# Performance work log

Hardware: AMD Instinct MI355X
Metric: run time of the kernel (lower is better)

The kernel has to match this reference:

```python
import jax, jax.numpy as jnp
import numpy as np

B, S, H, I, C = 1024, 512, 128, 1, 10


def _uniform(key, shape, fan):
    stdv = 1.0 / np.sqrt(fan)
    return jax.random.uniform(key, shape, jnp.float32, -stdv, stdv)


def setup_inputs() -> dict:
    key = jax.random.key(0)
    ks = jax.random.split(key, 16)
    return {
        "x": jax.random.normal(ks[0], (B, S), jnp.float32),
        "W_gx": _uniform(ks[1], (I, H), H),
        "W_gh": _uniform(ks[2], (H, H), H),
        "W_ix": _uniform(ks[3], (I, H), H),
        "W_ih": _uniform(ks[4], (H, H), H),
        "W_fx": _uniform(ks[5], (I, H), H),
        "W_fh": _uniform(ks[6], (H, H), H),
        "W_ox": _uniform(ks[7], (I, H), H),
        "W_oh": _uniform(ks[8], (H, H), H),
        "W_ph": _uniform(ks[9], (H, C), C),
        "b_g": _uniform(ks[10], (H,), 1),
        "b_i": _uniform(ks[11], (H,), 1),
        "b_f": _uniform(ks[12], (H,), 1),
        "b_o": _uniform(ks[13], (H,), 1),
        "b_p": _uniform(ks[14], (C,), 1),
    }


def reference(x, W_gx, W_gh, W_ix, W_ih, W_fx, W_fh, W_ox, W_oh, W_ph,
              b_g, b_i, b_f, b_o, b_p):
    Hd = W_gh.shape[0]
    # Fuse the four per-gate GEMMs into one (same math, concatenated weights).
    Wx = jnp.concatenate([W_gx, W_ix, W_fx, W_ox], axis=1)   # [I, 4H]
    Wh = jnp.concatenate([W_gh, W_ih, W_fh, W_oh], axis=1)   # [H, 4H]
    b = jnp.concatenate([b_g, b_i, b_f, b_o])                # [4H]
    # input_dim == 1: timestep t input is x[:, t:t+1] -> xs: [S, B, 1]
    xs = jnp.swapaxes(x[:, :, None], 0, 1)
    # Precompute all input projections in one big GEMM: [S, B, 4H]
    xp = xs @ Wx + b

    def step(carry, xp_t):
        h, c = carry
        gates = xp_t + h @ Wh                    # [B, 4H]
        g = jnp.tanh(gates[:, :Hd])
        i = jax.nn.sigmoid(gates[:, Hd:2 * Hd])
        f = jax.nn.sigmoid(gates[:, 2 * Hd:3 * Hd])
        o = jax.nn.sigmoid(gates[:, 3 * Hd:])
        c_t = g * i + c * f
        h_t = jnp.tanh(c_t) * o
        return (h_t, c_t), None

    h0 = jnp.zeros((x.shape[0], Hd), x.dtype)
    (h_last, _), _ = jax.lax.scan(step, (h0, h0), xp)
    return h_last @ W_ph + b_p                   # logits at final timestep
```

## Files before the change

kernel.cpp:

```cpp
#include <hip/hip_runtime.h>

#define S_LEN 512
#define H_DIM 128
#define C_DIM 10

typedef __attribute__((ext_vector_type(8))) short short8;
typedef __attribute__((ext_vector_type(4))) float f32x4;

__device__ __forceinline__ unsigned short f2bf(float f) {
    union { float f; unsigned u; } v; v.f = f;
    return (unsigned short)((v.u + 0x7FFFu + ((v.u >> 16) & 1u)) >> 16);
}

__device__ __forceinline__ float fast_sigmoid(float x) {
    float e = __builtin_amdgcn_exp2f(-1.4426950408889634f * x);
    return __builtin_amdgcn_rcpf(1.0f + e);
}
__device__ __forceinline__ float fast_tanh(float x) {
    float e = __builtin_amdgcn_exp2f(2.8853900817779268f * x);
    return 1.0f - 2.0f * __builtin_amdgcn_rcpf(e + 1.0f);
}

__global__ __launch_bounds__(512, 1) void lstm_fused(
    const float* __restrict__ x,
    const float* __restrict__ Wgx, const float* __restrict__ Wgh,
    const float* __restrict__ Wix, const float* __restrict__ Wih,
    const float* __restrict__ Wfx, const float* __restrict__ Wfh,
    const float* __restrict__ Wox, const float* __restrict__ Woh,
    const float* __restrict__ Wph,
    const float* __restrict__ bg, const float* __restrict__ bi,
    const float* __restrict__ bff, const float* __restrict__ bo,
    const float* __restrict__ bp,
    float* __restrict__ out)
{
    __shared__ float xr[4][516];
    __shared__ __attribute__((aligned(16))) unsigned short hb[2][512];
    __shared__ float hfin[4][H_DIM];

    const int tid  = threadIdx.x;
    const int lane = tid & 63;
    const int w    = tid >> 6;
    const int b0   = blockIdx.x * 4;

    {
        const float* xp = x + b0 * S_LEN;
        #pragma unroll
        for (int r = 0; r < 4; ++r) xr[r][tid] = xp[r * S_LEN + tid];
    }
    ((unsigned short*)hb)[tid] = 0;

    const int jl = lane & 15;
    const int kg = lane >> 4;
    const int j  = w * 16 + jl;

    const float* WhA[4] = { Wgh, Wih, Wfh, Woh };
    short8 bfrag[4][4];
    #pragma unroll
    for (int g = 0; g < 4; ++g) {
        #pragma unroll
        for (int kk = 0; kk < 4; ++kk) {
            const float* src = WhA[g] + (kk * 32 + kg * 8) * H_DIM + j;
            short8 v;
            #pragma unroll
            for (int e = 0; e < 8; ++e) v[e] = (short)f2bf(src[e * H_DIM]);
            bfrag[g][kk] = v;
        }
    }
    const float wxv[4] = { Wgx[j], Wix[j], Wfx[j], Wox[j] };
    const float bv[4]  = { bg[j],  bi[j],  bff[j], bo[j]  };

    const int abase = ((lane & 15) >> 2) * 16 + (lane >> 4) * 64;
    const int widx  = kg * 8 + ((j >> 3) & 3) * 32 + (j >> 5) * 128 + (j & 7);

    float cst  = 0.f;
    float hcur = 0.f;
    const f32x4 zf = { 0.f, 0.f, 0.f, 0.f };

    __syncthreads();

    unsigned short* const h0 = &hb[0][0];
    unsigned short* const h1 = &hb[1][0];

    auto step = [&](const unsigned short* src, unsigned short* dst, float xv) {
        float seed[4];
        #pragma unroll
        for (int g = 0; g < 4; ++g) seed[g] = __builtin_fmaf(xv, wxv[g], bv[g]);

        const char* base = (const char*)src + abase;
        short8 afr[4];
        #pragma unroll
        for (int kk = 0; kk < 4; ++kk)
            afr[kk] = *(const short8*)(base + kk * 256);

        f32x4 r[4][4];
        #pragma unroll
        for (int kk = 0; kk < 4; ++kk)
            #pragma unroll
            for (int g = 0; g < 4; ++g)
                r[g][kk] = __builtin_amdgcn_mfma_f32_16x16x32_bf16(
                               afr[kk], bfrag[g][kk], zf, 0, 0, 0);

        float pre[4];
        #pragma unroll
        for (int g = 0; g < 4; ++g) {
            const float t01 = r[g][0][0] + r[g][1][0];
            const float t23 = r[g][2][0] + (r[g][3][0] + seed[g]);
            pre[g] = t01 + t23;
        }

        const float tg = fast_tanh(pre[0]);
        const float si = fast_sigmoid(pre[1]);
        const float sf = fast_sigmoid(pre[2]);
        const float so = fast_sigmoid(pre[3]);
        const float cn = __builtin_fmaf(cst, sf, tg * si);
        cst  = cn;
        const float hn = fast_tanh(cn) * so;
        hcur = hn;
        unsigned pk;
        asm("v_cvt_pk_bf16_f32 %0, %1, %2" : "=v"(pk) : "v"(hn), "v"(hn));
        dst[widx] = (unsigned short)pk;
        __syncthreads();
    };

    for (int t4 = 0; t4 < S_LEN; t4 += 4) {
        const f32x4 xq = *(const f32x4*)&xr[kg][t4];
        step(h0, h1, xq[0]);
        step(h1, h0, xq[1]);
        step(h0, h1, xq[2]);
        step(h1, h0, xq[3]);
    }

    hfin[kg][j] = hcur;
    __syncthreads();

    if (tid < 4 * C_DIM) {
        const int b = tid / C_DIM, cc = tid % C_DIM;
        float s = bp[cc];
        #pragma unroll 8
        for (int k = 0; k < H_DIM; ++k) s += hfin[b][k] * Wph[k * C_DIM + cc];
        out[(b0 + b) * C_DIM + cc] = s;
    }
}

extern "C" void kernel_launch(void* const* d_in, const int* in_sizes, int n_in,
                              void* d_out, int out_size, void* d_ws, size_t ws_size,
                              hipStream_t stream) {
    const float* x   = (const float*)d_in[0];
    const float* Wgx = (const float*)d_in[1];
    const float* Wgh = (const float*)d_in[2];
    const float* Wix = (const float*)d_in[3];
    const float* Wih = (const float*)d_in[4];
    const float* Wfx = (const float*)d_in[5];
    const float* Wfh = (const float*)d_in[6];
    const float* Wox = (const float*)d_in[7];
    const float* Woh = (const float*)d_in[8];
    const float* Wph = (const float*)d_in[9];
    const float* bg  = (const float*)d_in[10];
    const float* bi  = (const float*)d_in[11];
    const float* bf  = (const float*)d_in[12];
    const float* bo  = (const float*)d_in[13];
    const float* bp  = (const float*)d_in[14];
    float* out = (float*)d_out;

    lstm_fused<<<dim3(256), dim3(512), 0, stream>>>(
        x, Wgx, Wgh, Wix, Wih, Wfx, Wfh, Wox, Woh, Wph,
        bg, bi, bf, bo, bp, out);
}
```

Before: 252.8 us.

## Process two independent 4-row batch groups per block to interleave recurrences

Each block now handles 8 batch rows as two independent 4-row LSTM recurrences that share one barrier per timestep. Their MFMA chains and gate math are interleaved to hide latency, and the grid shrinks to 128 blocks. Only lanes with (lane&3)==0 load real A fragments and the rest keep zero fragments. This is meant to halve the number of barriers per batch row and raise instruction-level parallelism within a step. In exchange there is more register pressure and fewer blocks (128 on a 256-CU part), so some CUs sit idle.

After: 412.0 us. +63.0%, slower.

```diff
diff --git a/kernel.cpp b/kernel.cpp
--- a/kernel.cpp
+++ b/kernel.cpp
@@ -21,7 +21,7 @@
     return 1.0f - 2.0f * __builtin_amdgcn_rcpf(e + 1.0f);
 }
 
-__global__ __launch_bounds__(512, 1) void lstm_fused(
+__global__ __launch_bounds__(512, 2) void lstm_fused(
     const float* __restrict__ x,
     const float* __restrict__ Wgx, const float* __restrict__ Wgh,
     const float* __restrict__ Wix, const float* __restrict__ Wih,
@@ -33,21 +33,22 @@
     const float* __restrict__ bp,
     float* __restrict__ out)
 {
-    __shared__ float xr[4][516];
-    __shared__ __attribute__((aligned(16))) unsigned short hb[2][512];
-    __shared__ float hfin[4][H_DIM];
+    __shared__ float xr[8][516];
+    __shared__ __attribute__((aligned(16))) unsigned short hb[2][2][512];
+    __shared__ float hfin[8][H_DIM];
 
     const int tid  = threadIdx.x;
     const int lane = tid & 63;
     const int w    = tid >> 6;
-    const int b0   = blockIdx.x * 4;
+    const int b0   = blockIdx.x * 8;
 
     {
         const float* xp = x + b0 * S_LEN;
         #pragma unroll
-        for (int r = 0; r < 4; ++r) xr[r][tid] = xp[r * S_LEN + tid];
-    }
-    ((unsigned short*)hb)[tid] = 0;
+        for (int r = 0; r < 8; ++r) xr[r][tid] = xp[r * S_LEN + tid];
+    }
+    ((unsigned*)hb)[tid]       = 0;
+    ((unsigned*)hb)[tid + 512] = 0;
 
     const int jl = lane & 15;
     const int kg = lane >> 4;
@@ -69,71 +70,112 @@
     const float wxv[4] = { Wgx[j], Wix[j], Wfx[j], Wox[j] };
     const float bv[4]  = { bg[j],  bi[j],  bff[j], bo[j]  };
 
-    const int abase = ((lane & 15) >> 2) * 16 + (lane >> 4) * 64;
-    const int widx  = kg * 8 + ((j >> 3) & 3) * 32 + (j >> 5) * 128 + (j & 7);
-
-    float cst  = 0.f;
-    float hcur = 0.f;
-    const f32x4 zf = { 0.f, 0.f, 0.f, 0.f };
+    const bool aActive = (lane & 3) == 0;
+    const int  abase   = (lane >> 2) * 16;
+    const int  widx    = kg * 8 + ((j >> 3) & 3) * 32 + (j >> 5) * 128 + (j & 7);
+
+    float cst0 = 0.f, cst1 = 0.f;
+    float hcv0 = 0.f, hcv1 = 0.f;
+
+    short8 af0[4], af1[4];
+    #pragma unroll
+    for (int kk = 0; kk < 4; ++kk) {
+        af0[kk] = short8{0,0,0,0,0,0,0,0};
+        af1[kk] = short8{0,0,0,0,0,0,0,0};
+    }
 
     __syncthreads();
 
-    unsigned short* const h0 = &hb[0][0];
-    unsigned short* const h1 = &hb[1][0];
-
-    auto step = [&](const unsigned short* src, unsigned short* dst, float xv) {
-        float seed[4];
-        #pragma unroll
-        for (int g = 0; g < 4; ++g) seed[g] = __builtin_fmaf(xv, wxv[g], bv[g]);
-
-        const char* base = (const char*)src + abase;
-        short8 afr[4];
-        #pragma unroll
-        for (int kk = 0; kk < 4; ++kk)
-            afr[kk] = *(const short8*)(base + kk * 256);
-
-        f32x4 r[4][4];
-        #pragma unroll
-        for (int kk = 0; kk < 4; ++kk)
-            #pragma unroll
-            for (int g = 0; g < 4; ++g)
-                r[g][kk] = __builtin_amdgcn_mfma_f32_16x16x32_bf16(
-                               afr[kk], bfrag[g][kk], zf, 0, 0, 0);
-
-        float pre[4];
+    unsigned short* const g0a = &hb[0][0][0];
+    unsigned short* const g0b = &hb[0][1][0];
+    unsigned short* const g1a = &hb[1][0][0];
+    unsigned short* const g1b = &hb[1][1][0];
+
+    auto iter = [&](const unsigned short* s0, unsigned short* d0,
+                    const unsigned short* s1, unsigned short* d1,
+                    float xv0, float xv1) {
+        if (aActive) {
+            const char* base0 = (const char*)s0 + abase;
+            const char* base1 = (const char*)s1 + abase;
+            #pragma unroll
+            for (int kk = 0; kk < 4; ++kk) {
+                af0[kk] = *(const short8*)(base0 + kk * 256);
+                af1[kk] = *(const short8*)(base1 + kk * 256);
+            }
+        }
+        float seed0[4], seed1[4];
         #pragma unroll
         for (int g = 0; g < 4; ++g) {
-            const float t01 = r[g][0][0] + r[g][1][0];
-            const float t23 = r[g][2][0] + (r[g][3][0] + seed[g]);
-            pre[g] = t01 + t23;
-        }
-
-        const float tg = fast_tanh(pre[0]);
-        const float si = fast_sigmoid(pre[1]);
-        const float sf = fast_sigmoid(pre[2]);
-        const float so = fast_sigmoid(pre[3]);
-        const float cn = __builtin_fmaf(cst, sf, tg * si);
-        cst  = cn;
-        const float hn = fast_tanh(cn) * so;
-        hcur = hn;
-        unsigned pk;
-        asm("v_cvt_pk_bf16_f32 %0, %1, %2" : "=v"(pk) : "v"(hn), "v"(hn));
-        dst[widx] = (unsigned short)pk;
+            seed0[g] = __builtin_fmaf(xv0, wxv[g], bv[g]);
+            seed1[g] = __builtin_fmaf(xv1, wxv[g], bv[g]);
+        }
+
+        const f32x4 zf = { 0.f, 0.f, 0.f, 0.f };
+        f32x4 a00[4], a01[4], a10[4], a11[4];
+        #pragma unroll
+        for (int g = 0; g < 4; ++g) {
+            a00[g] = __builtin_amdgcn_mfma_f32_16x16x32_bf16(af0[0], bfrag[g][0], zf, 0, 0, 0);
+            a01[g] = __builtin_amdgcn_mfma_f32_16x16x32_bf16(af0[2], bfrag[g][2], zf, 0, 0, 0);
+            a10[g] = __builtin_amdgcn_mfma_f32_16x16x32_bf16(af1[0], bfrag[g][0], zf, 0, 0, 0);
+            a11[g] = __builtin_amdgcn_mfma_f32_16x16x32_bf16(af1[2], bfrag[g][2], zf, 0, 0, 0);
+        }
+        #pragma unroll
+        for (int g = 0; g < 4; ++g) {
+            a00[g] = __builtin_amdgcn_mfma_f32_16x16x32_bf16(af0[1], bfrag[g][1], a00[g], 0, 0, 0);
+            a01[g] = __builtin_amdgcn_mfma_f32_16x16x32_bf16(af0[3], bfrag[g][3], a01[g], 0, 0, 0);
+            a10[g] = __builtin_amdgcn_mfma_f32_16x16x32_bf16(af1[1], bfrag[g][1], a10[g], 0, 0, 0);
+            a11[g] = __builtin_amdgcn_mfma_f32_16x16x32_bf16(af1[3], bfrag[g][3], a11[g], 0, 0, 0);
+        }
+
+        {
+            float pre[4];
+            #pragma unroll
+            for (int g = 0; g < 4; ++g) pre[g] = a00[g][0] + (a01[g][0] + seed0[g]);
+            const float tg = fast_tanh(pre[0]);
+            const float si = fast_sigmoid(pre[1]);
+            const float sf = fast_sigmoid(pre[2]);
+            const float so = fast_sigmoid(pre[3]);
+            const float cn = __builtin_fmaf(cst0, sf, tg * si);
+            cst0 = cn;
+            const float hn = fast_tanh(cn) * so;
+            hcv0 = hn;
+            unsigned pk;
+            asm("v_cvt_pk_bf16_f32 %0, %1, %2" : "=v"(pk) : "v"(hn), "v"(hn));
+            d0[widx] = (unsigned short)pk;
+        }
+        {
+            float pre[4];
+            #pragma unroll
+            for (int g = 0; g < 4; ++g) pre[g] = a10[g][0] + (a11[g][0] + seed1[g]);
+            const float tg = fast_tanh(pre[0]);
+            const float si = fast_sigmoid(pre[1]);
+            const float sf = fast_sigmoid(pre[2]);
+            const float so = fast_sigmoid(pre[3]);
+            const float cn = __builtin_fmaf(cst1, sf, tg * si);
+            cst1 = cn;
+            const float hn = fast_tanh(cn) * so;
+            hcv1 = hn;
+            unsigned pk;
+            asm("v_cvt_pk_bf16_f32 %0, %1, %2" : "=v"(pk) : "v"(hn), "v"(hn));
+            d1[widx] = (unsigned short)pk;
+        }
         __syncthreads();
     };
 
     for (int t4 = 0; t4 < S_LEN; t4 += 4) {
-        const f32x4 xq = *(const f32x4*)&xr[kg][t4];
-        step(h0, h1, xq[0]);
-        step(h1, h0, xq[1]);
-        step(h0, h1, xq[2]);
-        step(h1, h0, xq[3]);
-    }
-
-    hfin[kg][j] = hcur;
+        const f32x4 xq0 = *(const f32x4*)&xr[kg][t4];
+        const f32x4 xq1 = *(const f32x4*)&xr[4 + kg][t4];
+        iter(g0a, g0b, g1a, g1b, xq0[0], xq1[0]);
+        iter(g0b, g0a, g1b, g1a, xq0[1], xq1[1]);
+        iter(g0a, g0b, g1a, g1b, xq0[2], xq1[2]);
+        iter(g0b, g0a, g1b, g1a, xq0[3], xq1[3]);
+    }
+
+    hfin[kg][j]     = hcv0;
+    hfin[4 + kg][j] = hcv1;
     __syncthreads();
 
-    if (tid < 4 * C_DIM) {
+    if (tid < 8 * C_DIM) {
         const int b = tid / C_DIM, cc = tid % C_DIM;
         float s = bp[cc];
         #pragma unroll 8
@@ -162,7 +204,7 @@
     const float* bp  = (const float*)d_in[14];
     float* out = (float*)d_out;
 
-    lstm_fused<<<dim3(256), dim3(512), 0, stream>>>(
+    lstm_fused<<<dim3(128), dim3(512), 0, stream>>>(
         x, Wgx, Wgh, Wix, Wih, Wfx, Wfh, Wox, Woh, Wph,
         bg, bi, bf, bo, bp, out);
 }
```

## Chain MFMA accumulators, load only the needed A rows, prefetch x and raise priority

Applied to the files above, without the earlier changes.

The gate MFMAs now accumulate into two chained accumulators per gate, seeded with the input projection, instead of four independent MFMAs whose results are summed on the VALU. Only the lanes that own the used A rows (lane%4==0) read h from LDS, which cuts LDS traffic; the other lanes keep zero fragments. The x quad for the next iteration is prefetched, the elementwise tail runs under s_setprio 1, and launch bounds now allow two blocks per CU. Chaining the accumulators lengthens the MFMA dependency chain, and the change to launch bounds may limit registers.

Result: faster. 246.5 us (-2.5%).

```diff
diff --git a/kernel.cpp b/kernel.cpp
--- a/kernel.cpp
+++ b/kernel.cpp
@@ -21,7 +21,7 @@
     return 1.0f - 2.0f * __builtin_amdgcn_rcpf(e + 1.0f);
 }
 
-__global__ __launch_bounds__(512, 1) void lstm_fused(
+__global__ __launch_bounds__(512, 2) void lstm_fused(
     const float* __restrict__ x,
     const float* __restrict__ Wgx, const float* __restrict__ Wgh,
     const float* __restrict__ Wix, const float* __restrict__ Wih,
@@ -69,12 +69,16 @@
     const float wxv[4] = { Wgx[j], Wix[j], Wfx[j], Wox[j] };
     const float bv[4]  = { bg[j],  bi[j],  bff[j], bo[j]  };
 
-    const int abase = ((lane & 15) >> 2) * 16 + (lane >> 4) * 64;
-    const int widx  = kg * 8 + ((j >> 3) & 3) * 32 + (j >> 5) * 128 + (j & 7);
+    const bool aActive = (lane & 3) == 0;
+    const int  abase   = (lane >> 2) * 16;
+    const int  widx    = kg * 8 + ((j >> 3) & 3) * 32 + (j >> 5) * 128 + (j & 7);
 
     float cst  = 0.f;
     float hcur = 0.f;
-    const f32x4 zf = { 0.f, 0.f, 0.f, 0.f };
+
+    short8 afr[4];
+    #pragma unroll
+    for (int kk = 0; kk < 4; ++kk) afr[kk] = short8{0,0,0,0,0,0,0,0};
 
     __syncthreads();
 
@@ -82,36 +86,39 @@
     unsigned short* const h1 = &hb[1][0];
 
     auto step = [&](const unsigned short* src, unsigned short* dst, float xv) {
-        float seed[4];
-        #pragma unroll
-        for (int g = 0; g < 4; ++g) seed[g] = __builtin_fmaf(xv, wxv[g], bv[g]);
-
-        const char* base = (const char*)src + abase;
-        short8 afr[4];
-        #pragma unroll
-        for (int kk = 0; kk < 4; ++kk)
-            afr[kk] = *(const short8*)(base + kk * 256);
-
-        f32x4 r[4][4];
-        #pragma unroll
-        for (int kk = 0; kk < 4; ++kk)
+        if (aActive) {
+            const char* base = (const char*)src + abase;
             #pragma unroll
-            for (int g = 0; g < 4; ++g)
-                r[g][kk] = __builtin_amdgcn_mfma_f32_16x16x32_bf16(
-                               afr[kk], bfrag[g][kk], zf, 0, 0, 0);
-
-        float pre[4];
+            for (int kk = 0; kk < 4; ++kk)
+                afr[kk] = *(const short8*)(base + kk * 256);
+        }
+        f32x4 a0[4], a1[4];
         #pragma unroll
         for (int g = 0; g < 4; ++g) {
-            const float t01 = r[g][0][0] + r[g][1][0];
-            const float t23 = r[g][2][0] + (r[g][3][0] + seed[g]);
-            pre[g] = t01 + t23;
+            const float sd = __builtin_fmaf(xv, wxv[g], bv[g]);
+            a0[g] = f32x4{ sd, sd, sd, sd };
+            a1[g] = f32x4{ 0.f, 0.f, 0.f, 0.f };
+        }
+        #pragma unroll
+        for (int g = 0; g < 4; ++g) {
+            a0[g] = __builtin_amdgcn_mfma_f32_16x16x32_bf16(afr[0], bfrag[g][0], a0[g], 0, 0, 0);
+            a1[g] = __builtin_amdgcn_mfma_f32_16x16x32_bf16(afr[2], bfrag[g][2], a1[g], 0, 0, 0);
+        }
+        #pragma unroll
+        for (int g = 0; g < 4; ++g) {
+            a0[g] = __builtin_amdgcn_mfma_f32_16x16x32_bf16(afr[1], bfrag[g][1], a0[g], 0, 0, 0);
+            a1[g] = __builtin_amdgcn_mfma_f32_16x16x32_bf16(afr[3], bfrag[g][3], a1[g], 0, 0, 0);
         }
 
-        const float tg = fast_tanh(pre[0]);
-        const float si = fast_sigmoid(pre[1]);
-        const float sf = fast_sigmoid(pre[2]);
-        const float so = fast_sigmoid(pre[3]);
+        __builtin_amdgcn_s_setprio(1);
+        const float pg = a0[0][0] + a1[0][0];
+        const float pi = a0[1][0] + a1[1][0];
+        const float pf = a0[2][0] + a1[2][0];
+        const float po = a0[3][0] + a1[3][0];
+        const float tg = fast_tanh(pg);
+        const float si = fast_sigmoid(pi);
+        const float sf = fast_sigmoid(pf);
+        const float so = fast_sigmoid(po);
         const float cn = __builtin_fmaf(cst, sf, tg * si);
         cst  = cn;
         const float hn = fast_tanh(cn) * so;
@@ -119,15 +126,19 @@
         unsigned pk;
         asm("v_cvt_pk_bf16_f32 %0, %1, %2" : "=v"(pk) : "v"(hn), "v"(hn));
         dst[widx] = (unsigned short)pk;
+        __builtin_amdgcn_s_setprio(0);
         __syncthreads();
     };
 
+    f32x4 xq = *(const f32x4*)&xr[kg][0];
     for (int t4 = 0; t4 < S_LEN; t4 += 4) {
-        const f32x4 xq = *(const f32x4*)&xr[kg][t4];
         step(h0, h1, xq[0]);
+        const int nt = (t4 + 4) & (S_LEN - 1);
+        const f32x4 xnq = *(const f32x4*)&xr[kg][nt];
         step(h1, h0, xq[1]);
         step(h0, h1, xq[2]);
         step(h1, h0, xq[3]);
+        xq = xnq;
     }
 
     hfin[kg][j] = hcur;
```
